# Kernel optimization log

Measured on AMD Instinct MI355X. Metric: run time of the kernel, lower is better.

Reference implementation:

```python
import jax, jax.numpy as jnp
import numpy as np


def setup_inputs() -> dict:
    key = jax.random.key(0)
    k1, k2, k3, k4, k5 = jax.random.split(key, 5)
    b, c, k, h, w = 8, 512, 19, 128, 128
    x = jax.random.normal(k1, (b, c, h, w), dtype=jnp.float32)
    # mask_conv: 1x1 conv ichn->ochn (weight [k, c], bias [k])
    Wm = jax.random.normal(k2, (k, c), dtype=jnp.float32) * (1.0 / np.sqrt(c))
    bm = jax.random.normal(k3, (k,), dtype=jnp.float32) * 0.02
    # filter_conv: grouped 1x1 conv, groups=k -> per-class [c_out, c_in] matmul
    Wf = jax.random.normal(k4, (k, c, c), dtype=jnp.float32) * (1.0 / np.sqrt(c))
    bf = jax.random.normal(k5, (k, c), dtype=jnp.float32) * 0.02
    return {"x": x, "Wm": Wm, "bm": bm, "Wf": Wf, "bf": bf}


def reference(x, Wm, bm, Wf, bf):
    b, c, h, w = x.shape
    k = Wm.shape[0]
    # mask_conv (1x1) + sigmoid -> [b, k, h, w]
    pre_mask = jnp.einsum('bchw,kc->bkhw', x, Wm) + bm[None, :, None, None]
    mask = jax.nn.sigmoid(pre_mask)
    # masked pooling: bmm(mask [b,k,hw], feat [b,hw,c]) / (h*w) -> [b, k, c]
    class_feat = jnp.einsum('bkhw,bchw->bkc', mask, x) / (h * w)
    # grouped 1x1 filter_conv: per class k, [c_out, c_in] GEMM on class_feat
    filters = jnp.einsum('koc,bkc->bko', Wf, class_feat) + bf[None, :, :]  # [b, k, c]
    # per-sample dynamic 1x1 conv (groups=b) == batched GEMM over channels
    pred = jnp.einsum('bkc,bchw->bkhw', filters, x)
    return pred
```

## Files before the change

### kernel.cpp

```cpp
#include <hip/hip_runtime.h>
#include <math.h>

#define BB 8
#define CC 512
#define KK 19
#define HWHW 16384
#define INV_HW (1.0f/16384.0f)

typedef __attribute__((ext_vector_type(8))) short bf16x8;
typedef __attribute__((ext_vector_type(4))) short s16x4;
typedef __attribute__((ext_vector_type(4))) float f32x4;

__device__ __forceinline__ unsigned short f2bf(float f) {
    unsigned int u = __float_as_uint(f);
    u = (u + 0x7fffu + ((u >> 16) & 1u)) >> 16;
    return (unsigned short)u;
}

__device__ __forceinline__ unsigned int pk_bf16(float a, float b) {
    unsigned int r;
    asm("v_cvt_pk_bf16_f32 %0, %1, %2" : "=v"(r) : "v"(a), "v"(b));
    return r;
}

__global__ __launch_bounds__(512, 2) void k_s12(const float* __restrict__ x,
                                                const float* __restrict__ Wm,
                                                const float* __restrict__ bm,
                                                float* __restrict__ cf_part,
                                                unsigned short* __restrict__ xt4g) {
    __shared__ short wm[20 * CC];
    __shared__ short xf[8 * 8192];
    __shared__ short mlds[20 * 128];
    const int tid = threadIdx.x;
    const int b = blockIdx.x >> 7;
    const int pt = blockIdx.x & 127;
    const float* xb = x + ((size_t)b * CC) * HWHW + (pt << 7);

    const int wv = tid >> 6, ln = tid & 63;
    const int lm = ln & 15, q = ln >> 4;

    const int cr0 = (tid >> 5) << 2;
    const int pA = (tid & 31) << 2;
    const int cg = tid >> 5;
    const float* sbase = xb + (size_t)cr0 * HWHW + pA;

    float4 Fa[4], Fb[4], Fc[4];
#pragma unroll
    for (int j = 0; j < 4; ++j) Fa[j] = *(const float4*)(sbase + (size_t)j * HWHW);
#pragma unroll
    for (int j = 0; j < 4; ++j) Fb[j] = *(const float4*)(sbase + (size_t)(64 + j) * HWHW);

    for (int u = tid; u < 20 * 128; u += 512) {
        const int k = u >> 7;
        const int c4 = (u & 127) << 2;
        float4 w = {0.f, 0.f, 0.f, 0.f};
        if (k < KK) w = *(const float4*)(Wm + k * CC + c4);
        s16x4 v = { (short)f2bf(w.x), (short)f2bf(w.y), (short)f2bf(w.z), (short)f2bf(w.w) };
        *(s16x4*)&wm[(k << 9) + (((c4 >> 3) ^ (k & 7)) << 3) + (c4 & 7)] = v;
    }
    if (tid < 16)
        *(uint4*)&mlds[(19 << 7) + (tid << 3)] = make_uint4(0u, 0u, 0u, 0u);

    const f32x4 zz = {0.f, 0.f, 0.f, 0.f};
    f32x4 acc[2];
    acc[0] = zz; acc[1] = zz;

    unsigned short* t4fix = xt4g + ((size_t)((b << 7) | pt) << 16);

#pragma unroll
    for (int cs = 0; cs < 8; ++cs) {
        const float4* cur = (cs % 3 == 0) ? Fa : ((cs % 3 == 1) ? Fb : Fc);
        float4* nxt = ((cs + 2) % 3 == 0) ? Fa : (((cs + 2) % 3 == 1) ? Fb : Fc);
        if (cs < 6) {
            const size_t co = (size_t)((cs + 2) << 6) * HWHW;
#pragma unroll
            for (int j = 0; j < 4; ++j)
                nxt[j] = *(const float4*)(sbase + co + (size_t)j * HWHW);
        }
        short* xts = &xf[cs << 13];
        {
            const float* G0 = (const float*)&cur[0];
            const float* G1 = (const float*)&cur[1];
            const float* G2 = (const float*)&cur[2];
            const float* G3 = (const float*)&cur[3];
#pragma unroll
            for (int jj = 0; jj < 4; ++jj) {
                const int pr = pA + jj;
                uint2 v = make_uint2(pk_bf16(G0[jj], G1[jj]), pk_bf16(G2[jj], G3[jj]));
                *(uint2*)&xts[(pr << 6) + (((cg >> 1) ^ (pr & 7)) << 3) + ((cg & 1) << 2)] = v;
            }
        }
        __syncthreads();
#pragma unroll
        for (int ks = 0; ks < 2; ++ks) {
            const int gch = (cs << 3) + (ks << 2) + q;
            const int m1 = (lm < 3) ? (16 + lm) : 19;
            bf16x8 a0 = *(const bf16x8*)&wm[(lm << 9) + ((gch ^ (lm & 7)) << 3)];
            bf16x8 a1 = *(const bf16x8*)&wm[(m1 << 9) + ((gch ^ (m1 & 7)) << 3)];
            const int lch = (ks << 2) + q;
            const int pr = (wv << 4) + lm;
            bf16x8 bv = *(const bf16x8*)&xts[(pr << 6) + ((lch ^ (pr & 7)) << 3)];
            acc[0] = __builtin_amdgcn_mfma_f32_16x16x32_bf16(a0, bv, acc[0], 0, 0, 0);
            acc[1] = __builtin_amdgcn_mfma_f32_16x16x32_bf16(a1, bv, acc[1], 0, 0, 0);
        }
        {
            unsigned short* t4 = t4fix + ((size_t)cs << 13);
#pragma unroll
            for (int r = 0; r < 2; ++r) {
                uint4 v = *(const uint4*)&xts[(r << 12) + (tid << 3)];
                *(uint4*)(t4 + (r << 12) + (tid << 3)) = v;
            }
        }
        __syncthreads();
    }

    {
        const int prow = (wv << 4) + lm;
#pragma unroll
        for (int mt = 0; mt < 2; ++mt)
#pragma unroll
            for (int r = 0; r < 4; ++r) {
                const int k = (mt << 4) + (q << 2) + r;
                if (k < KK) {
                    const float t = acc[mt][r] + bm[k];
                    const unsigned short mv = f2bf(1.0f / (1.0f + __expf(-t)));
                    mlds[(k << 7) + (((prow >> 3) ^ (k & 7)) << 3) + (prow & 7)] =
                        (short)mv;
                }
            }
    }
    __syncthreads();

    f32x4 pacc[2][4];
#pragma unroll
    for (int mt = 0; mt < 2; ++mt)
#pragma unroll
        for (int ct = 0; ct < 4; ++ct) pacc[mt][ct] = zz;

    const short* xw = &xf[wv << 13];
    const int m1 = (lm < 3) ? (16 + lm) : 19;
#pragma unroll
    for (int kp = 0; kp < 4; ++kp) {
        const int pg = (kp << 2) + q;
        bf16x8 a0 = *(const bf16x8*)&mlds[(lm << 7) + ((pg ^ (lm & 7)) << 3)];
        bf16x8 a1 = *(const bf16x8*)&mlds[(m1 << 7) + ((pg ^ (m1 & 7)) << 3)];
#pragma unroll
        for (int ct = 0; ct < 4; ++ct) {
            const int cl = (ct << 4) + lm;
            short e[8];
#pragma unroll
            for (int i = 0; i < 8; ++i) {
                const int p = (kp << 5) + (q << 3) + i;
                e[i] = xw[(p << 6) + (((cl >> 3) ^ (p & 7)) << 3) + (cl & 7)];
            }
            bf16x8 bv = {e[0], e[1], e[2], e[3], e[4], e[5], e[6], e[7]};
            pacc[0][ct] = __builtin_amdgcn_mfma_f32_16x16x32_bf16(a0, bv, pacc[0][ct], 0, 0, 0);
            pacc[1][ct] = __builtin_amdgcn_mfma_f32_16x16x32_bf16(a1, bv, pacc[1][ct], 0, 0, 0);
        }
    }

    float* dst = cf_part + ((size_t)pt * BB + b) * KK * CC;
#pragma unroll
    for (int mt = 0; mt < 2; ++mt)
#pragma unroll
        for (int r = 0; r < 4; ++r) {
            const int k = (mt << 4) + (q << 2) + r;
            if (k < KK) {
#pragma unroll
                for (int ct = 0; ct < 4; ++ct)
                    dst[k * CC + (wv << 6) + (ct << 4) + lm] = pacc[mt][ct][r];
            }
        }
}

__global__ __launch_bounds__(256) void k_s2r(const float* __restrict__ part,
                                             float* __restrict__ cf) {
    const int i = blockIdx.x * 256 + threadIdx.x;
    if (i >= BB * KK * CC) return;
    const int b = i / (KK * CC);
    const int rem = i - b * (KK * CC);
    float sum = 0.0f;
#pragma unroll 8
    for (int pt = 0; pt < 128; ++pt)
        sum += part[((size_t)pt * BB + b) * KK * CC + rem];
    cf[i] = sum * INV_HW;
}

__global__ __launch_bounds__(256) void k_filters(const float* __restrict__ Wf,
                                                 const float* __restrict__ bf,
                                                 const float* __restrict__ cf,
                                                 float* __restrict__ fil) {
    const int blk = blockIdx.x;
    const int k = blk >> 7;
    const int o = ((blk & 127) << 2) + (threadIdx.x >> 6);
    const int lane = threadIdx.x & 63;
    const float* wrow = Wf + ((size_t)k * CC + o) * CC;

    float acc[BB];
#pragma unroll
    for (int b = 0; b < BB; ++b) acc[b] = 0.0f;
#pragma unroll
    for (int j = 0; j < CC / 64; ++j) {
        const int c = lane + (j << 6);
        const float wv = wrow[c];
#pragma unroll
        for (int b = 0; b < BB; ++b)
            acc[b] += wv * cf[((size_t)b * KK + k) * CC + c];
    }
#pragma unroll
    for (int b = 0; b < BB; ++b) {
#pragma unroll
        for (int off = 32; off > 0; off >>= 1)
            acc[b] += __shfl_down(acc[b], off, 64);
    }
    if (lane == 0) {
        const float bias = bf[k * CC + o];
#pragma unroll
        for (int b = 0; b < BB; ++b)
            fil[((size_t)b * KK + k) * CC + o] = acc[b] + bias;
    }
}

__global__ __launch_bounds__(256, 3) void k_s4(const unsigned short* __restrict__ xt4g,
                                               const float* __restrict__ fil,
                                               float* __restrict__ out) {
    __shared__ short wm[20 * CC];
    __shared__ short xt[2][128 * 64];
    const int tid = threadIdx.x;
    const int b = blockIdx.x >> 7;
    const int pt = blockIdx.x & 127;
    const int p0 = pt << 7;
    const float* fb = fil + ((size_t)b * KK) * CC;
    const unsigned short* tb = xt4g + ((size_t)((b << 7) | pt) << 16);

    for (int u = tid; u < 20 * 128; u += 256) {
        const int k = u >> 7;
        const int c4 = (u & 127) << 2;
        float4 w = {0.f, 0.f, 0.f, 0.f};
        if (k < KK) w = *(const float4*)(fb + k * CC + c4);
        s16x4 v = { (short)f2bf(w.x), (short)f2bf(w.y), (short)f2bf(w.z), (short)f2bf(w.w) };
        *(s16x4*)&wm[(k << 9) + (((c4 >> 3) ^ (k & 7)) << 3) + (c4 & 7)] = v;
    }

    const int wv = tid >> 6, ln = tid & 63;
    const int lm = ln & 15, q = ln >> 4;
    const f32x4 zz = {0.f, 0.f, 0.f, 0.f};
    f32x4 acc[2][2];
    acc[0][0] = zz; acc[0][1] = zz; acc[1][0] = zz; acc[1][1] = zz;

    uint4 Ta[4], Tb4[4];
#pragma unroll
    for (int r = 0; r < 4; ++r)
        Ta[r] = *(const uint4*)(tb + (r << 11) + (tid << 3));

#pragma unroll
    for (int cs = 0; cs < 8; ++cs) {
        const uint4* cur = (cs & 1) ? Tb4 : Ta;
        uint4* nxt = (cs & 1) ? Ta : Tb4;
        if (cs < 7) {
#pragma unroll
            for (int r = 0; r < 4; ++r)
                nxt[r] = *(const uint4*)(tb + ((size_t)(cs + 1) << 13) + (r << 11) + (tid << 3));
        }
        short* xts = (short*)xt[cs & 1];
#pragma unroll
        for (int r = 0; r < 4; ++r)
            *(uint4*)&xts[(r << 11) + (tid << 3)] = cur[r];
        asm volatile("s_waitcnt lgkmcnt(0)" ::: "memory");
        __builtin_amdgcn_s_barrier();
        asm volatile("" ::: "memory");
#pragma unroll
        for (int ks = 0; ks < 2; ++ks) {
            const int gch = (cs << 3) + (ks << 2) + q;
            const int m1 = (lm < 3) ? (16 + lm) : 19;
            bf16x8 a0 = *(const bf16x8*)&wm[(lm << 9) + ((gch ^ (lm & 7)) << 3)];
            bf16x8 a1 = *(const bf16x8*)&wm[(m1 << 9) + ((gch ^ (m1 & 7)) << 3)];
            const int lch = (ks << 2) + q;
#pragma unroll
            for (int nt = 0; nt < 2; ++nt) {
                const int pr = (((wv << 1) + nt) << 4) + lm;
                bf16x8 bv = *(const bf16x8*)&xts[(pr << 6) + ((lch ^ (pr & 7)) << 3)];
                acc[0][nt] = __builtin_amdgcn_mfma_f32_16x16x32_bf16(a0, bv, acc[0][nt], 0, 0, 0);
                acc[1][nt] = __builtin_amdgcn_mfma_f32_16x16x32_bf16(a1, bv, acc[1][nt], 0, 0, 0);
            }
        }
    }

    float* ob = out + ((size_t)b * KK) * HWHW + p0;
#pragma unroll
    for (int mt = 0; mt < 2; ++mt)
#pragma unroll
        for (int r = 0; r < 4; ++r) {
            const int k = (mt << 4) + (q << 2) + r;
            if (k < KK) {
#pragma unroll
                for (int nt = 0; nt < 2; ++nt) {
                    const int p = (((wv << 1) + nt) << 4) + lm;
                    ob[(size_t)k * HWHW + p] = acc[mt][nt][r];
                }
            }
        }
}

extern "C" void kernel_launch(void* const* d_in, const int* in_sizes, int n_in,
                              void* d_out, int out_size, void* d_ws, size_t ws_size,
                              hipStream_t stream) {
    const float* x  = (const float*)d_in[0];
    const float* Wm = (const float*)d_in[1];
    const float* bm = (const float*)d_in[2];
    const float* Wf = (const float*)d_in[3];
    const float* bf = (const float*)d_in[4];
    float* out = (float*)d_out;

    char* p = (char*)d_ws;
    float* cf_part = (float*)p;                 p += (size_t)128 * BB * KK * CC * 4;
    float* cf  = (float*)p;                     p += (size_t)BB * KK * CC * 4;
    float* fil = (float*)p;                     p += (size_t)BB * KK * CC * 4;
    unsigned short* xt4g = (unsigned short*)p;

    k_s12<<<1024, 512, 0, stream>>>(x, Wm, bm, cf_part, xt4g);
    k_s2r<<<(BB * KK * CC + 255) / 256, 256, 0, stream>>>(cf_part, cf);
    k_filters<<<KK * 128, 256, 0, stream>>>(Wf, bf, cf, fil);
    k_s4<<<1024, 256, 0, stream>>>(xt4g, fil, out);
}
```

Before: 449.9 us.

## Process four pixel tiles per block with double-buffered LDS and fewer partials

The mask/pooling kernel now loops over four pixel tiles per block. It keeps the pooled class-feature accumulators in registers across tiles and only double-buffers x chunks in LDS instead of holding all eight channel slices. The pooling pass reloads the bf16 tile it just wrote to global scratch rather than reading it from LDS. This shrinks the partial-sum buffer and its reduction by four times and cuts LDS use per block. The cost is extra global reads, more barriers, and only 256 blocks of serial work per CU.

```diff
diff --git a/kernel.cpp b/kernel.cpp
--- a/kernel.cpp
+++ b/kernel.cpp
@@ -23,32 +23,20 @@
     return r;
 }
 
-__global__ __launch_bounds__(512, 2) void k_s12(const float* __restrict__ x,
+__global__ __launch_bounds__(512, 4) void k_s12(const float* __restrict__ x,
                                                 const float* __restrict__ Wm,
                                                 const float* __restrict__ bm,
                                                 float* __restrict__ cf_part,
                                                 unsigned short* __restrict__ xt4g) {
     __shared__ short wm[20 * CC];
-    __shared__ short xf[8 * 8192];
+    __shared__ short xc[2][8192];
     __shared__ short mlds[20 * 128];
     const int tid = threadIdx.x;
-    const int b = blockIdx.x >> 7;
-    const int pt = blockIdx.x & 127;
-    const float* xb = x + ((size_t)b * CC) * HWHW + (pt << 7);
+    const int b = blockIdx.x >> 5;
+    const int ptg = blockIdx.x & 31;
 
     const int wv = tid >> 6, ln = tid & 63;
     const int lm = ln & 15, q = ln >> 4;
-
-    const int cr0 = (tid >> 5) << 2;
-    const int pA = (tid & 31) << 2;
-    const int cg = tid >> 5;
-    const float* sbase = xb + (size_t)cr0 * HWHW + pA;
-
-    float4 Fa[4], Fb[4], Fc[4];
-#pragma unroll
-    for (int j = 0; j < 4; ++j) Fa[j] = *(const float4*)(sbase + (size_t)j * HWHW);
-#pragma unroll
-    for (int j = 0; j < 4; ++j) Fb[j] = *(const float4*)(sbase + (size_t)(64 + j) * HWHW);
 
     for (int u = tid; u < 20 * 128; u += 512) {
         const int k = u >> 7;
@@ -62,115 +50,137 @@
         *(uint4*)&mlds[(19 << 7) + (tid << 3)] = make_uint4(0u, 0u, 0u, 0u);
 
     const f32x4 zz = {0.f, 0.f, 0.f, 0.f};
-    f32x4 acc[2];
-    acc[0] = zz; acc[1] = zz;
-
-    unsigned short* t4fix = xt4g + ((size_t)((b << 7) | pt) << 16);
-
+    f32x4 pacc[8];
+#pragma unroll
+    for (int cs = 0; cs < 8; ++cs) pacc[cs] = zz;
+
+    const int cr0 = (tid >> 5) << 2;
+    const int pA  = (tid & 31) << 2;
+    const int cg  = tid >> 5;
+    const int kt = wv >> 2, ct = wv & 3;
+    const int m1 = (lm < 3) ? (16 + lm) : 19;
+
+#pragma unroll
+    for (int t = 0; t < 4; ++t) {
+        const int pt = (ptg << 2) + t;
+        const float* sbase = x + ((size_t)b * CC + cr0) * HWHW + (pt << 7) + pA;
+        unsigned short* t4fix = xt4g + ((size_t)((b << 7) | pt) << 16);
+
+        f32x4 acc0 = zz, acc1 = zz;
+
+        float4 Fa[4], Fb[4];
+#pragma unroll
+        for (int j = 0; j < 4; ++j) Fa[j] = *(const float4*)(sbase + (size_t)j * HWHW);
+
+#pragma unroll
+        for (int cs = 0; cs < 8; ++cs) {
+            const float4* cur = (cs & 1) ? Fb : Fa;
+            float4* nxt = (cs & 1) ? Fa : Fb;
+            if (cs < 7) {
+                const size_t co = (size_t)((cs + 1) << 6) * HWHW;
+#pragma unroll
+                for (int j = 0; j < 4; ++j)
+                    nxt[j] = *(const float4*)(sbase + co + (size_t)j * HWHW);
+            }
+            short* xts = (short*)xc[cs & 1];
+            {
+                const float* G0 = (const float*)&cur[0];
+                const float* G1 = (const float*)&cur[1];
+                const float* G2 = (const float*)&cur[2];
+                const float* G3 = (const float*)&cur[3];
+#pragma unroll
+                for (int jj = 0; jj < 4; ++jj) {
+                    const int pr = pA + jj;
+                    uint2 v = make_uint2(pk_bf16(G0[jj], G1[jj]), pk_bf16(G2[jj], G3[jj]));
+                    *(uint2*)&xts[(pr << 6) + (((cg >> 1) ^ (pr & 7)) << 3) + ((cg & 1) << 2)] = v;
+                }
+            }
+            __syncthreads();
+#pragma unroll
+            for (int ks = 0; ks < 2; ++ks) {
+                const int gch = (cs << 3) + (ks << 2) + q;
+                bf16x8 a0 = *(const bf16x8*)&wm[(lm << 9) + ((gch ^ (lm & 7)) << 3)];
+                bf16x8 a1 = *(const bf16x8*)&wm[(m1 << 9) + ((gch ^ (m1 & 7)) << 3)];
+                const int lch = (ks << 2) + q;
+                const int pr = (wv << 4) + lm;
+                bf16x8 bv = *(const bf16x8*)&xts[(pr << 6) + ((lch ^ (pr & 7)) << 3)];
+                acc0 = __builtin_amdgcn_mfma_f32_16x16x32_bf16(a0, bv, acc0, 0, 0, 0);
+                acc1 = __builtin_amdgcn_mfma_f32_16x16x32_bf16(a1, bv, acc1, 0, 0, 0);
+            }
+            {
+                unsigned short* t4 = t4fix + ((size_t)cs << 13);
+#pragma unroll
+                for (int r = 0; r < 2; ++r) {
+                    uint4 v = *(const uint4*)&xts[(r << 12) + (tid << 3)];
+                    *(uint4*)(t4 + (r << 12) + (tid << 3)) = v;
+                }
+            }
+            __syncthreads();
+        }
+
+        {
+            const int prow = (wv << 4) + lm;
+#pragma unroll
+            for (int mt = 0; mt < 2; ++mt) {
+                const f32x4 a = mt ? acc1 : acc0;
+#pragma unroll
+                for (int r = 0; r < 4; ++r) {
+                    const int k = (mt << 4) + (q << 2) + r;
+                    if (k < KK) {
+                        const float tt = a[r] + bm[k];
+                        mlds[(k << 7) + (((prow >> 3) ^ (k & 7)) << 3) + (prow & 7)] =
+                            (short)f2bf(1.0f / (1.0f + __expf(-tt)));
+                    }
+                }
+            }
+        }
+        __syncthreads();
+
+        uint4 Pa[2], Pb[2];
+        Pa[0] = *(const uint4*)(t4fix + (tid << 4));
+        Pa[1] = *(const uint4*)(t4fix + (tid << 4) + 8);
+#pragma unroll
+        for (int cs = 0; cs < 8; ++cs) {
+            const uint4* curP = (cs & 1) ? Pb : Pa;
+            uint4* nxtP = (cs & 1) ? Pa : Pb;
+            if (cs < 7) {
+                const unsigned short* tp = t4fix + ((size_t)(cs + 1) << 13);
+                nxtP[0] = *(const uint4*)(tp + (tid << 4));
+                nxtP[1] = *(const uint4*)(tp + (tid << 4) + 8);
+            }
+            short* xts = (short*)xc[cs & 1];
+            *(uint4*)&xts[(tid << 4)] = curP[0];
+            *(uint4*)&xts[(tid << 4) + 8] = curP[1];
+            __syncthreads();
+            const int cl = (ct << 4) + lm;
+#pragma unroll
+            for (int kp = 0; kp < 4; ++kp) {
+                const int pg = (kp << 2) + q;
+                bf16x8 a = (kt == 0)
+                    ? *(const bf16x8*)&mlds[(lm << 7) + ((pg ^ (lm & 7)) << 3)]
+                    : *(const bf16x8*)&mlds[(m1 << 7) + ((pg ^ (m1 & 7)) << 3)];
+                short e[8];
+#pragma unroll
+                for (int i = 0; i < 8; ++i) {
+                    const int p = (kp << 5) + (q << 3) + i;
+                    e[i] = xts[(p << 6) + (((cl >> 3) ^ (p & 7)) << 3) + (cl & 7)];
+                }
+                bf16x8 bv = {e[0], e[1], e[2], e[3], e[4], e[5], e[6], e[7]};
+                pacc[cs] = __builtin_amdgcn_mfma_f32_16x16x32_bf16(a, bv, pacc[cs], 0, 0, 0);
+            }
+            __syncthreads();
+        }
+    }
+
+    float* dst = cf_part + ((size_t)ptg * BB + b) * KK * CC;
 #pragma unroll
     for (int cs = 0; cs < 8; ++cs) {
-        const float4* cur = (cs % 3 == 0) ? Fa : ((cs % 3 == 1) ? Fb : Fc);
-        float4* nxt = ((cs + 2) % 3 == 0) ? Fa : (((cs + 2) % 3 == 1) ? Fb : Fc);
-        if (cs < 6) {
-            const size_t co = (size_t)((cs + 2) << 6) * HWHW;
-#pragma unroll
-            for (int j = 0; j < 4; ++j)
-                nxt[j] = *(const float4*)(sbase + co + (size_t)j * HWHW);
-        }
-        short* xts = &xf[cs << 13];
-        {
-            const float* G0 = (const float*)&cur[0];
-            const float* G1 = (const float*)&cur[1];
-            const float* G2 = (const float*)&cur[2];
-            const float* G3 = (const float*)&cur[3];
-#pragma unroll
-            for (int jj = 0; jj < 4; ++jj) {
-                const int pr = pA + jj;
-                uint2 v = make_uint2(pk_bf16(G0[jj], G1[jj]), pk_bf16(G2[jj], G3[jj]));
-                *(uint2*)&xts[(pr << 6) + (((cg >> 1) ^ (pr & 7)) << 3) + ((cg & 1) << 2)] = v;
-            }
-        }
-        __syncthreads();
-#pragma unroll
-        for (int ks = 0; ks < 2; ++ks) {
-            const int gch = (cs << 3) + (ks << 2) + q;
-            const int m1 = (lm < 3) ? (16 + lm) : 19;
-            bf16x8 a0 = *(const bf16x8*)&wm[(lm << 9) + ((gch ^ (lm & 7)) << 3)];
-            bf16x8 a1 = *(const bf16x8*)&wm[(m1 << 9) + ((gch ^ (m1 & 7)) << 3)];
-            const int lch = (ks << 2) + q;
-            const int pr = (wv << 4) + lm;
-            bf16x8 bv = *(const bf16x8*)&xts[(pr << 6) + ((lch ^ (pr & 7)) << 3)];
-            acc[0] = __builtin_amdgcn_mfma_f32_16x16x32_bf16(a0, bv, acc[0], 0, 0, 0);
-            acc[1] = __builtin_amdgcn_mfma_f32_16x16x32_bf16(a1, bv, acc[1], 0, 0, 0);
-        }
-        {
-            unsigned short* t4 = t4fix + ((size_t)cs << 13);
-#pragma unroll
-            for (int r = 0; r < 2; ++r) {
-                uint4 v = *(const uint4*)&xts[(r << 12) + (tid << 3)];
-                *(uint4*)(t4 + (r << 12) + (tid << 3)) = v;
-            }
-        }
-        __syncthreads();
-    }
-
-    {
-        const int prow = (wv << 4) + lm;
-#pragma unroll
-        for (int mt = 0; mt < 2; ++mt)
-#pragma unroll
-            for (int r = 0; r < 4; ++r) {
-                const int k = (mt << 4) + (q << 2) + r;
-                if (k < KK) {
-                    const float t = acc[mt][r] + bm[k];
-                    const unsigned short mv = f2bf(1.0f / (1.0f + __expf(-t)));
-                    mlds[(k << 7) + (((prow >> 3) ^ (k & 7)) << 3) + (prow & 7)] =
-                        (short)mv;
-                }
-            }
-    }
-    __syncthreads();
-
-    f32x4 pacc[2][4];
-#pragma unroll
-    for (int mt = 0; mt < 2; ++mt)
-#pragma unroll
-        for (int ct = 0; ct < 4; ++ct) pacc[mt][ct] = zz;
-
-    const short* xw = &xf[wv << 13];
-    const int m1 = (lm < 3) ? (16 + lm) : 19;
-#pragma unroll
-    for (int kp = 0; kp < 4; ++kp) {
-        const int pg = (kp << 2) + q;
-        bf16x8 a0 = *(const bf16x8*)&mlds[(lm << 7) + ((pg ^ (lm & 7)) << 3)];
-        bf16x8 a1 = *(const bf16x8*)&mlds[(m1 << 7) + ((pg ^ (m1 & 7)) << 3)];
-#pragma unroll
-        for (int ct = 0; ct < 4; ++ct) {
-            const int cl = (ct << 4) + lm;
-            short e[8];
-#pragma unroll
-            for (int i = 0; i < 8; ++i) {
-                const int p = (kp << 5) + (q << 3) + i;
-                e[i] = xw[(p << 6) + (((cl >> 3) ^ (p & 7)) << 3) + (cl & 7)];
-            }
-            bf16x8 bv = {e[0], e[1], e[2], e[3], e[4], e[5], e[6], e[7]};
-            pacc[0][ct] = __builtin_amdgcn_mfma_f32_16x16x32_bf16(a0, bv, pacc[0][ct], 0, 0, 0);
-            pacc[1][ct] = __builtin_amdgcn_mfma_f32_16x16x32_bf16(a1, bv, pacc[1][ct], 0, 0, 0);
-        }
-    }
-
-    float* dst = cf_part + ((size_t)pt * BB + b) * KK * CC;
-#pragma unroll
-    for (int mt = 0; mt < 2; ++mt)
 #pragma unroll
         for (int r = 0; r < 4; ++r) {
-            const int k = (mt << 4) + (q << 2) + r;
-            if (k < KK) {
-#pragma unroll
-                for (int ct = 0; ct < 4; ++ct)
-                    dst[k * CC + (wv << 6) + (ct << 4) + lm] = pacc[mt][ct][r];
-            }
-        }
+            const int k = (kt << 4) + (q << 2) + r;
+            if (k < KK) dst[k * CC + (cs << 6) + (ct << 4) + lm] = pacc[cs][r];
+        }
+    }
 }
 
 __global__ __launch_bounds__(256) void k_s2r(const float* __restrict__ part,
@@ -181,7 +191,7 @@
     const int rem = i - b * (KK * CC);
     float sum = 0.0f;
 #pragma unroll 8
-    for (int pt = 0; pt < 128; ++pt)
+    for (int pt = 0; pt < 32; ++pt)
         sum += part[((size_t)pt * BB + b) * KK * CC + rem];
     cf[i] = sum * INV_HW;
 }
@@ -313,12 +323,12 @@
     float* out = (float*)d_out;
 
     char* p = (char*)d_ws;
-    float* cf_part = (float*)p;                 p += (size_t)128 * BB * KK * CC * 4;
+    float* cf_part = (float*)p;                 p += (size_t)32 * BB * KK * CC * 4;
     float* cf  = (float*)p;                     p += (size_t)BB * KK * CC * 4;
     float* fil = (float*)p;                     p += (size_t)BB * KK * CC * 4;
     unsigned short* xt4g = (unsigned short*)p;
 
-    k_s12<<<1024, 512, 0, stream>>>(x, Wm, bm, cf_part, xt4g);
+    k_s12<<<256, 512, 0, stream>>>(x, Wm, bm, cf_part, xt4g);
     k_s2r<<<(BB * KK * CC + 255) / 256, 256, 0, stream>>>(cf_part, cf);
     k_filters<<<KK * 128, 256, 0, stream>>>(Wf, bf, cf, fil);
     k_s4<<<1024, 256, 0, stream>>>(xt4g, fil, out);
```

Result: slower. 491.2 us (+9.2%).
